# Kernel optimization log

Measured on AMD Instinct MI355X. Metric: run time of the kernel, lower is better.

Reference implementation:

```python
import jax, jax.numpy as jnp
import numpy as np
import math

E = 2048         # n_embd
H = 16           # num query head pairs (num_heads)
HKV = 8          # num_kv_heads
NREP = H // HKV  # 2
HD = E // H // 2 # head_dim = 64
DEPTH = 12
LAMBDA_INIT = 0.8 - 0.6 * math.exp(-0.3 * DEPTH)
EPS = 1e-6


def setup_inputs() -> dict:
    key = jax.random.key(0)
    ks = jax.random.split(key, 10)
    s = lambda fan_in: 1.0 / np.sqrt(fan_in)
    return {
        "x": jax.random.normal(ks[0], (2, 2048, E), jnp.float32),
        "Wq": jax.random.normal(ks[1], (E, E), jnp.float32) * s(E),
        "Wk": jax.random.normal(ks[2], (E, E // NREP), jnp.float32) * s(E),
        "Wv": jax.random.normal(ks[3], (E, E // NREP), jnp.float32) * s(E),
        "Wo": jax.random.normal(ks[4], (E, E), jnp.float32) * s(E),
        "lam_q1": jax.random.normal(ks[5], (HD,), jnp.float32) * 0.1,
        "lam_k1": jax.random.normal(ks[6], (HD,), jnp.float32) * 0.1,
        "lam_q2": jax.random.normal(ks[7], (HD,), jnp.float32) * 0.1,
        "lam_k2": jax.random.normal(ks[8], (HD,), jnp.float32) * 0.1,
        "g": jnp.ones((2 * HD,), jnp.float32),  # RMSNorm weight
    }


def _rotary(x, cos, sin):
    # x: [B, T, nh, HD]; cos/sin: [T, HD//2]
    d = x.shape[-1] // 2
    x1, x2 = x[..., :d], x[..., d:]
    c = cos[None, :, None, :]
    si = sin[None, :, None, :]
    return jnp.concatenate([x1 * c + x2 * si, -x1 * si + x2 * c], axis=-1)


def reference(x, Wq, Wk, Wv, Wo, lam_q1, lam_k1, lam_q2, lam_k2, g):
    B, T, _ = x.shape
    q = (x @ Wq).reshape(B, T, 2 * H, HD)
    k = (x @ Wk).reshape(B, T, 2 * HKV, HD)
    v = (x @ Wv).reshape(B, T, HKV, 2 * HD)

    inv_freq = 1.0 / (10000.0 ** (jnp.arange(0, HD, 2, dtype=jnp.float32) / HD))
    freqs = jnp.arange(T, dtype=jnp.float32)[:, None] * inv_freq[None, :]
    cos, sin = jnp.cos(freqs), jnp.sin(freqs)
    q = _rotary(q, cos, sin)
    k = _rotary(k, cos, sin)

    q = jnp.transpose(q, (0, 2, 1, 3)) * (HD ** -0.5)   # [B, 2H, T, HD]
    k = jnp.repeat(jnp.transpose(k, (0, 2, 1, 3)), NREP, axis=1)  # [B, 2H, T, HD]
    v = jnp.repeat(jnp.transpose(v, (0, 2, 1, 3)), NREP, axis=1)  # [B, H, T, 2HD]

    scores = jnp.einsum('bhtd,bhsd->bhts', q, k)
    scores = jnp.nan_to_num(scores)
    mask = jnp.triu(jnp.full((T, T), -jnp.inf, scores.dtype), 1)
    scores = scores + mask
    p = jax.nn.softmax(scores.astype(jnp.float32), axis=-1).astype(scores.dtype)

    lam1 = jnp.exp(jnp.sum(lam_q1 * lam_k1))
    lam2 = jnp.exp(jnp.sum(lam_q2 * lam_k2))
    lam = lam1 - lam2 + LAMBDA_INIT

    p = p.reshape(B, H, 2, T, T)
    diff = p[:, :, 0] - lam * p[:, :, 1]               # [B, H, T, T]
    attn = jnp.einsum('bhts,bhsd->bhtd', diff, v)      # [B, H, T, 2HD]

    # RMSNorm over last dim (2*HD)
    attn = attn * jax.lax.rsqrt(jnp.mean(attn * attn, axis=-1, keepdims=True) + EPS) * g
    attn = attn * (1.0 - LAMBDA_INIT)
    attn = jnp.transpose(attn, (0, 2, 1, 3)).reshape(B, T, E)
    return attn @ Wo
```

## Files before the change

### kernel.cpp

```cpp
#include <hip/hip_runtime.h>

#define T_SEQ 2048

typedef __bf16 bf16x8 __attribute__((ext_vector_type(8)));
typedef float f32x4 __attribute__((ext_vector_type(4)));
typedef unsigned short u16;

__device__ __forceinline__ u16 f2b(float f) {
  unsigned u = __float_as_uint(f);
  unsigned r = 0x7fffu + ((u >> 16) & 1u);
  return (u16)((u + r) >> 16);
}
__device__ __forceinline__ float b2f(u16 v) {
  return __uint_as_float(((unsigned)v) << 16);
}
__device__ __forceinline__ f32x4 mfma16(bf16x8 a, bf16x8 b, f32x4 c) {
  return __builtin_amdgcn_mfma_f32_16x16x32_bf16(a, b, c, 0, 0, 0);
}
__device__ __forceinline__ unsigned pkhi(float lo, float hi) {
  return __builtin_amdgcn_perm(__float_as_uint(hi), __float_as_uint(lo), 0x07060302u);
}
#if defined(__has_builtin)
#if __has_builtin(__builtin_amdgcn_exp2f)
#define HAVE_RAW_EXP2 1
#endif
#endif
__device__ __forceinline__ float exp2r(float x) {
#ifdef HAVE_RAW_EXP2
  return __builtin_amdgcn_exp2f(x);
#else
  float r;
  asm("v_exp_f32 %0, %1" : "=v"(r) : "v"(x));
  return r;
#endif
}
__device__ __forceinline__ void glds16(const void* g, void* s) {
  __builtin_amdgcn_global_load_lds(
      (const __attribute__((address_space(1))) void*)(uintptr_t)g,
      (__attribute__((address_space(3))) void*)(unsigned)(uintptr_t)s, 16, 0, 0);
}

__global__ void lam_kernel(const float* __restrict__ q1, const float* __restrict__ k1,
                           const float* __restrict__ q2, const float* __restrict__ k2,
                           float* __restrict__ outp) {
  int l = threadIdx.x;
  float a = q1[l] * k1[l];
  float c = q2[l] * k2[l];
  #pragma unroll
  for (int off = 32; off > 0; off >>= 1) {
    a += __shfl_down(a, off);
    c += __shfl_down(c, off);
  }
  if (l == 0) outp[0] = expf(a) - expf(c) + 0.7836057665316244f;
}

__global__ __launch_bounds__(256) void convert_kernel(const float* __restrict__ in,
                                                      u16* __restrict__ outp, int n) {
  int i = (blockIdx.x * 256 + threadIdx.x) * 4;
  if (i >= n) return;
  float4 v = *(const float4*)(in + i);
  ushort4 pk;
  pk.x = f2b(v.x); pk.y = f2b(v.y); pk.z = f2b(v.z); pk.w = f2b(v.w);
  *(ushort4*)(outp + i) = pk;
}

__global__ __launch_bounds__(256) void transposeW_kernel(const float* __restrict__ Wq,
                                                         const float* __restrict__ Wk,
                                                         const float* __restrict__ Wv,
                                                         const float* __restrict__ Wo,
                                                         u16* __restrict__ outp) {
  __shared__ float tile[32][33];
  const int ro0 = blockIdx.y * 32;
  const int r0 = blockIdx.x * 32;
  const float* src; int C, cbase;
  if (ro0 < 2048)      { src = Wq; C = 2048; cbase = 0; }
  else if (ro0 < 3072) { src = Wk; C = 1024; cbase = 2048; }
  else if (ro0 < 4096) { src = Wv; C = 1024; cbase = 3072; }
  else                 { src = Wo; C = 2048; cbase = 4096; }
  const int cs0 = ro0 - cbase;
  const int tx = threadIdx.x & 31, ty = threadIdx.x >> 5;
  #pragma unroll
  for (int k2 = 0; k2 < 4; k2++)
    tile[ty * 4 + k2][tx] = src[(size_t)(r0 + ty * 4 + k2) * C + cs0 + tx];
  __syncthreads();
  #pragma unroll
  for (int k2 = 0; k2 < 4; k2++)
    outp[(size_t)(ro0 + ty * 4 + k2) * 2048 + r0 + tx] = f2b(tile[tx][ty * 4 + k2]);
}

template <bool OUT_BF16>
__global__ __launch_bounds__(256) void gemm128_kernel(const u16* __restrict__ A,
                                                      const u16* __restrict__ BT,
                                                      void* __restrict__ C, int N, int K) {
  __shared__ alignas(16) u16 As[128 * 64];
  __shared__ alignas(16) u16 Bs[128 * 64];
  const int tid = threadIdx.x, w = tid >> 6, lane = tid & 63;
  const int l15 = lane & 15, quad = lane >> 4;
  const int m0 = blockIdx.y * 128, n0 = blockIdx.x * 128;
  const int wm = (w >> 1) * 64, wn = (w & 1) * 64;
  const int lr = lane >> 3, slot = lane & 7, csw = slot ^ lr;
  f32x4 acc[4][4];
  #pragma unroll
  for (int mt = 0; mt < 4; mt++)
    #pragma unroll
    for (int nt = 0; nt < 4; nt++) acc[mt][nt] = (f32x4){0.f, 0.f, 0.f, 0.f};
  const u16* Ag = A + (size_t)(m0 + w * 32 + lr) * K + csw * 8;
  const u16* Bg = BT + (size_t)(n0 + w * 32 + lr) * K + csw * 8;
  u16* Asd = As + (w * 32) * 64;
  u16* Bsd = Bs + (w * 32) * 64;
  for (int kt = 0; kt < K; kt += 64) {
    #pragma unroll
    for (int i = 0; i < 4; i++) {
      glds16(Ag + kt + (size_t)(i * 8) * K, Asd + i * 512);
      glds16(Bg + kt + (size_t)(i * 8) * K, Bsd + i * 512);
    }
    __syncthreads();
    #pragma unroll
    for (int kk = 0; kk < 2; kk++) {
      bf16x8 am[4], bn[4];
      #pragma unroll
      for (int t = 0; t < 4; t++) {
        const int ra = wm + t * 16 + l15;
        am[t] = *(const bf16x8*)&As[ra * 64 + (((kk * 4 + quad) ^ (ra & 7)) << 3)];
        const int rb = wn + t * 16 + l15;
        bn[t] = *(const bf16x8*)&Bs[rb * 64 + (((kk * 4 + quad) ^ (rb & 7)) << 3)];
      }
      #pragma unroll
      for (int mt = 0; mt < 4; mt++)
        #pragma unroll
        for (int nt = 0; nt < 4; nt++) acc[mt][nt] = mfma16(am[mt], bn[nt], acc[mt][nt]);
    }
    __syncthreads();
  }
  const int row = m0 + wm + quad * 4;
  #pragma unroll
  for (int mt = 0; mt < 4; mt++) {
    #pragma unroll
    for (int nt = 0; nt < 4; nt++) {
      const int col = n0 + wn + nt * 16 + l15;
      #pragma unroll
      for (int rr = 0; rr < 4; rr++) {
        if (OUT_BF16)
          ((u16*)C)[(size_t)(row + mt * 16 + rr) * N + col] = f2b(acc[mt][nt][rr]);
        else
          ((float*)C)[(size_t)(row + mt * 16 + rr) * N + col] = acc[mt][nt][rr];
      }
    }
  }
}

#define STAGE_HALF(TILE, ROLE, BUF)                                                     \
  do {                                                                                  \
    const u16* sp_ = ((ROLE) == 0 || (ROLE) == 3 ? Ag : Bg) +                           \
                     (size_t)((ROLE) >= 2 ? 128 : 0) * K + (size_t)(TILE) * 64;         \
    u16* dp_ = ((ROLE) == 0 || (ROLE) == 3 ? &As[BUF][0] : &Bs[BUF][0]) +               \
               (((ROLE) >= 2 ? 128 : 0) + w * 8) * 64;                                  \
    glds16(sp_, dp_);                                                                   \
    glds16(sp_ + (size_t)64 * K, dp_ + 4096);                                           \
  } while (0)

#define PHASE(I, J, BUF, NEWA, NEWB, BN, STILE, SROLE, SBUF, DOVM)                      \
  do {                                                                                  \
    if (NEWA) {                                                                         \
      _Pragma("unroll") for (int u_ = 0; u_ < 4; u_++) {                                \
        const int ar_ = ((I) * 4 + u_) * 32 + wm * 16 + l15;                            \
        _Pragma("unroll") for (int kk_ = 0; kk_ < 2; kk_++)                             \
            am[u_][kk_] = *(const bf16x8*)&As[BUF][ar_ * 64 +                           \
                              (((kk_ * 4 + quad) ^ (ar_ & 7)) << 3)];                   \
      }                                                                                 \
    }                                                                                   \
    if (NEWB) {                                                                         \
      _Pragma("unroll") for (int v_ = 0; v_ < 2; v_++) {                                \
        const int br_ = ((J) * 2 + v_) * 64 + wn * 16 + l15;                            \
        _Pragma("unroll") for (int kk_ = 0; kk_ < 2; kk_++)                             \
            BN[v_][kk_] = *(const bf16x8*)&Bs[BUF][br_ * 64 +                           \
                              (((kk_ * 4 + quad) ^ (br_ & 7)) << 3)];                   \
      }                                                                                 \
    }                                                                                   \
    STAGE_HALF(STILE, SROLE, SBUF);                                                     \
    __builtin_amdgcn_s_barrier();                                                       \
    asm volatile("s_waitcnt lgkmcnt(0)" ::: "memory");                                  \
    __builtin_amdgcn_sched_barrier(0);                                                  \
    __builtin_amdgcn_s_setprio(1);                                                      \
    _Pragma("unroll") for (int u_ = 0; u_ < 4; u_++)                                    \
        _Pragma("unroll") for (int v_ = 0; v_ < 2; v_++) {                              \
      acc[(I) * 4 + u_][(J) * 2 + v_] =                                                 \
          mfma16(am[u_][0], BN[v_][0], acc[(I) * 4 + u_][(J) * 2 + v_]);                \
      acc[(I) * 4 + u_][(J) * 2 + v_] =                                                 \
          mfma16(am[u_][1], BN[v_][1], acc[(I) * 4 + u_][(J) * 2 + v_]);                \
    }                                                                                   \
    __builtin_amdgcn_s_setprio(0);                                                      \
    if (DOVM) asm volatile("s_waitcnt vmcnt(6)" ::: "memory");                          \
    __builtin_amdgcn_s_barrier();                                                       \
  } while (0)

__global__ __launch_bounds__(512, 2) void gemm256_kernel(const u16* __restrict__ A,
                                                         const u16* __restrict__ BT,
                                                         u16* __restrict__ C, int N, int K) {
  __shared__ alignas(16) u16 As[2][256 * 64];
  __shared__ alignas(16) u16 Bs[2][256 * 64];
  const int tid = threadIdx.x, w = tid >> 6, lane = tid & 63;
  const int l15 = lane & 15, quad = lane >> 4;
  const int wm = w >> 2, wn = w & 3;
  const int lr = lane >> 3, slot = lane & 7, csw = slot ^ lr;
  const int m0 = blockIdx.y * 256, n0 = blockIdx.x * 256;
  const int nkt = K >> 6;

  f32x4 acc[8][4];
  #pragma unroll
  for (int r = 0; r < 8; r++)
    #pragma unroll
    for (int s = 0; s < 4; s++) acc[r][s] = (f32x4){0.f, 0.f, 0.f, 0.f};

  const u16* Ag = A + (size_t)(m0 + w * 8 + lr) * K + csw * 8;
  const u16* Bg = BT + (size_t)(n0 + w * 8 + lr) * K + csw * 8;

  bf16x8 am[4][2], bn0[2][2], bn1[2][2];

  STAGE_HALF(0, 0, 0); STAGE_HALF(0, 1, 0); STAGE_HALF(0, 2, 0); STAGE_HALF(0, 3, 0);
  STAGE_HALF(1, 0, 1); STAGE_HALF(1, 1, 1); STAGE_HALF(1, 2, 1);
  asm volatile("s_waitcnt vmcnt(6)" ::: "memory");
  __builtin_amdgcn_s_barrier();

  #pragma unroll 1
  for (int t = 0; t < nkt; t += 2) {
    PHASE(0, 0, 0, 1, 1, bn0, t + 1, 3, 1, 0);
    PHASE(0, 1, 0, 0, 1, bn1, t + 2, 0, 0, 0);
    PHASE(1, 0, 0, 1, 0, bn0, t + 2, 1, 0, 0);
    PHASE(1, 1, 0, 0, 0, bn1, t + 2, 2, 0, 1);
    PHASE(0, 0, 1, 1, 1, bn0, t + 2, 3, 0, 0);
    PHASE(0, 1, 1, 0, 1, bn1, t + 3, 0, 1, 0);
    PHASE(1, 0, 1, 1, 0, bn0, t + 3, 1, 1, 0);
    PHASE(1, 1, 1, 0, 0, bn1, t + 3, 2, 1, 1);
  }

  const int crow = m0 + wm * 16 + quad * 4;
  const int ccol = n0 + wn * 16 + l15;
  #pragma unroll
  for (int r = 0; r < 8; r++)
    #pragma unroll
    for (int s = 0; s < 4; s++)
      #pragma unroll
      for (int rr = 0; rr < 4; rr++)
        C[(size_t)(crow + r * 32 + rr) * N + ccol + s * 64] = f2b(acc[r][s][rr]);
}

__global__ __launch_bounds__(256) void rotab_kernel(float* __restrict__ ct,
                                                    float* __restrict__ st) {
  int idx = blockIdx.x * 256 + threadIdx.x;
  int i = idx & 31, t = idx >> 5;
  float invf = exp2f(-(float)i * 0.4152410118609203f);
  float ang = (float)t * invf;
  ct[idx] = cosf(ang);
  st[idx] = sinf(ang);
}

__global__ __launch_bounds__(256) void rotary_kernel(const u16* __restrict__ qkv,
                                                     const float* __restrict__ ct,
                                                     const float* __restrict__ st,
                                                     u16* __restrict__ Qb,
                                                     u16* __restrict__ Kb, float qscale) {
  int idx = blockIdx.x * 256 + threadIdx.x;
  int i4 = (idx & 7) * 4;
  int bt = (idx >> 3) & 4095;
  int hh = idx >> 15;
  int t = bt & (T_SEQ - 1), b = bt >> 11;
  bool isq = hh < 32;
  int col = isq ? hh * 64 : 2048 + (hh - 32) * 64;
  size_t inb = (size_t)bt * 4096 + col + i4;
  ushort4 xa = *(const ushort4*)(qkv + inb);
  ushort4 xb = *(const ushort4*)(qkv + inb + 32);
  float4 c4 = *(const float4*)(ct + t * 32 + i4);
  float4 s4 = *(const float4*)(st + t * 32 + i4);
  float scale = isq ? qscale : 1.0f;
  ushort4 o1, o2;
  {
    float x1 = b2f(xa.x), x2 = b2f(xb.x);
    o1.x = f2b((x1 * c4.x + x2 * s4.x) * scale);
    o2.x = f2b((x2 * c4.x - x1 * s4.x) * scale);
  }
  {
    float x1 = b2f(xa.y), x2 = b2f(xb.y);
    o1.y = f2b((x1 * c4.y + x2 * s4.y) * scale);
    o2.y = f2b((x2 * c4.y - x1 * s4.y) * scale);
  }
  {
    float x1 = b2f(xa.z), x2 = b2f(xb.z);
    o1.z = f2b((x1 * c4.z + x2 * s4.z) * scale);
    o2.z = f2b((x2 * c4.z - x1 * s4.z) * scale);
  }
  {
    float x1 = b2f(xa.w), x2 = b2f(xb.w);
    o1.w = f2b((x1 * c4.w + x2 * s4.w) * scale);
    o2.w = f2b((x2 * c4.w - x1 * s4.w) * scale);
  }
  u16* outp = isq ? (Qb + (size_t)(b * 32 + hh) * (T_SEQ * 64))
                  : (Kb + (size_t)(b * 16 + hh - 32) * (T_SEQ * 64));
  size_t ob = (size_t)t * 64 + i4;
  *(ushort4*)(outp + ob) = o1;
  *(ushort4*)(outp + ob + 32) = o2;
}

__global__ __launch_bounds__(256) void vtrans_kernel(const u16* __restrict__ qkv,
                                                     u16* __restrict__ outp) {
  __shared__ unsigned tile[32][33];
  int bh = blockIdx.z;
  int t0 = blockIdx.x * 32, dv0 = blockIdx.y * 32;
  int tx = threadIdx.x & 31, ty = threadIdx.x >> 5;
  int bt_base = (bh >> 3) * T_SEQ;
  int col = 3072 + (bh & 7) * 128 + dv0 + tx;
  #pragma unroll
  for (int k2 = 0; k2 < 4; k2++)
    tile[ty * 4 + k2][tx] = qkv[(size_t)(bt_base + t0 + ty * 4 + k2) * 4096 + col];
  __syncthreads();
  const int stile = t0 >> 6;
  const int sold = (t0 & 63) + tx;
  const int slo = sold & 31, hb = sold >> 5;
  const int sp = hb * 32 + ((slo >> 2) & 3) * 8 + ((slo >> 4) & 1) * 4 + (slo & 3);
  #pragma unroll
  for (int k2 = 0; k2 < 4; k2++) {
    int dv = dv0 + ty * 4 + k2;
    outp[(((size_t)bh * 32 + stile) * 128 + dv) * 64 + sp] = (u16)tile[tx][ty * 4 + k2];
  }
}

__global__ __launch_bounds__(256) void attn_kernel(const u16* __restrict__ Qb,
                                                   const u16* __restrict__ Kb,
                                                   const u16* __restrict__ Vt,
                                                   const float* __restrict__ lamp,
                                                   const float* __restrict__ g,
                                                   u16* __restrict__ attn_out) {
  __shared__ alignas(16) char smem[49152];
  u16* const Ks0 = (u16*)smem;
  u16* const Vs0 = (u16*)(smem + 16384);
  u16* const Psb = (u16*)smem;
  const int pr = blockIdx.x;
  const int bh = blockIdx.y;
  const int b = bh >> 4, h = bh & 15;
  const int tid = threadIdx.x, w = tid >> 6, lane = tid & 63;
  const int l15 = lane & 15, quad = lane >> 4;
  const int lr = lane >> 3, slot = lane & 7, csw = slot ^ lr;
  const float lam = lamp[0];

  const u16* Kg = Kb + (size_t)(b * 16 + h) * (T_SEQ * 64) + (w * 16 + lr) * 64 + csw * 8;
  const u16* Vg = Vt + (size_t)(b * 8 + (h >> 1)) * (T_SEQ * 128) + w * 2048 + lr * 64 + csw * 8;
  u16* kd[2] = {Ks0 + w * 1024, Ks0 + 4096 + w * 1024};
  u16* vd[2] = {Vs0 + w * 2048, Vs0 + 8192 + w * 2048};

  #pragma unroll 1
  for (int half = 0; half < 2; half++) {
    const int tt = half ? 31 - pr : pr;
    const int qb = tt * 64 + w * 16;
    const int qglob = qb + l15;

    bf16x8 qf[2][2];
    #pragma unroll
    for (int e = 0; e < 2; e++)
      #pragma unroll
      for (int kk = 0; kk < 2; kk++)
        qf[e][kk] = *(const bf16x8*)&Qb[((size_t)(b * 32 + 2 * h + e) * T_SEQ + qb + l15) * 64 +
                                        kk * 32 + quad * 8];

    f32x4 o[2][8];
    float lsum[2] = {0.f, 0.f};
    #pragma unroll
    for (int e = 0; e < 2; e++)
      #pragma unroll
      for (int nt = 0; nt < 8; nt++) o[e][nt] = (f32x4){0.f, 0.f, 0.f, 0.f};

    {
      glds16(Kg, kd[0]); glds16(Kg + 512, kd[0] + 512);
      glds16(Vg, vd[0]); glds16(Vg + 512, vd[0] + 512);
      glds16(Vg + 1024, vd[0] + 1024); glds16(Vg + 1536, vd[0] + 1536);
    }
    __syncthreads();

    #pragma unroll 1
    for (int st = 0; st <= tt; st++) {
      const int buf = st & 1;
      const u16* Ksb = Ks0 + buf * 4096;
      const u16* Vsb = Vs0 + buf * 8192;
      if (st < tt) {
        const u16* kp = Kg + (size_t)(st + 1) * 4096;
        const u16* vp = Vg + (size_t)(st + 1) * 8192;
        glds16(kp, kd[buf ^ 1]); glds16(kp + 512, kd[buf ^ 1] + 512);
        glds16(vp, vd[buf ^ 1]); glds16(vp + 512, vd[buf ^ 1] + 512);
        glds16(vp + 1024, vd[buf ^ 1] + 1024); glds16(vp + 1536, vd[buf ^ 1] + 1536);
      }

      bf16x8 kf[4][2];
      #pragma unroll
      for (int j = 0; j < 4; j++) {
        const int rk = j * 16 + l15;
        #pragma unroll
        for (int kk = 0; kk < 2; kk++)
          kf[j][kk] = *(const bf16x8*)&Ksb[rk * 64 + (((kk * 4 + quad) ^ (rk & 7)) << 3)];
      }

      bf16x8 pa[2][2];
      #pragma unroll
      for (int e = 0; e < 2; e++) {
        f32x4 sc[4];
        __builtin_amdgcn_s_setprio(1);
        #pragma unroll
        for (int j = 0; j < 4; j++) {
          f32x4 z = {0.f, 0.f, 0.f, 0.f};
          z = mfma16(kf[j][0], qf[e][0], z);
          sc[j] = mfma16(kf[j][1], qf[e][1], z);
        }
        __builtin_amdgcn_s_setprio(0);
        if (st == tt) {
          #pragma unroll
          for (int j = 0; j < 4; j++) {
            int srow = st * 64 + j * 16 + quad * 4;
            #pragma unroll
            for (int rr = 0; rr < 4; rr++)
              if (srow + rr > qglob) sc[j][rr] = -1e30f;
          }
        }
        float ls = 0.f;
        union { unsigned u[8]; bf16x8 v[2]; } pk;
        #pragma unroll
        for (int j = 0; j < 4; j++) {
          #pragma unroll
          for (int rr = 0; rr < 4; rr++) {
            float p = exp2r(sc[j][rr]);
            sc[j][rr] = p;
            ls += p;
          }
          pk.u[j * 2] = pkhi(sc[j][0], sc[j][1]);
          pk.u[j * 2 + 1] = pkhi(sc[j][2], sc[j][3]);
        }
        pa[e][0] = pk.v[0];
        pa[e][1] = pk.v[1];
        lsum[e] += ls;
      }
      __builtin_amdgcn_s_setprio(1);
      #pragma unroll
      for (int nt = 0; nt < 8; nt++) {
        const int rv = nt * 16 + l15;
        bf16x8 vf0 = *(const bf16x8*)&Vsb[rv * 64 + ((quad ^ (rv & 7)) << 3)];
        bf16x8 vf1 = *(const bf16x8*)&Vsb[rv * 64 + (((4 + quad) ^ (rv & 7)) << 3)];
        o[0][nt] = mfma16(vf0, pa[0][0], o[0][nt]);
        o[0][nt] = mfma16(vf1, pa[0][1], o[0][nt]);
        o[1][nt] = mfma16(vf0, pa[1][0], o[1][nt]);
        o[1][nt] = mfma16(vf1, pa[1][1], o[1][nt]);
      }
      __builtin_amdgcn_s_setprio(0);
      __syncthreads();
    }

    float l0 = lsum[0], l1 = lsum[1];
    l0 += __shfl_xor(l0, 16); l0 += __shfl_xor(l0, 32);
    l1 += __shfl_xor(l1, 16); l1 += __shfl_xor(l1, 32);
    const float il0 = 1.f / l0, il1 = lam / l1;
    float ssq = 0.f;
    #pragma unroll
    for (int nt = 0; nt < 8; nt++)
      #pragma unroll
      for (int rr = 0; rr < 4; rr++) {
        float v = o[0][nt][rr] * il0 - o[1][nt][rr] * il1;
        o[0][nt][rr] = v;
        ssq += v * v;
      }
    ssq += __shfl_xor(ssq, 16);
    ssq += __shfl_xor(ssq, 32);
    const float rsc = rsqrtf(ssq * (1.f / 128.f) + 1e-6f) * 0.2163942334683756f;
    #pragma unroll
    for (int nt = 0; nt < 8; nt++) {
      float4 gv = *(const float4*)&g[nt * 16 + quad * 4];
      uint2 pk;
      pk.x = (unsigned)f2b(o[0][nt][0] * rsc * gv.x) |
             ((unsigned)f2b(o[0][nt][1] * rsc * gv.y) << 16);
      pk.y = (unsigned)f2b(o[0][nt][2] * rsc * gv.z) |
             ((unsigned)f2b(o[0][nt][3] * rsc * gv.w) << 16);
      *(uint2*)&Psb[(w * 16 + l15) * 136 + nt * 16 + quad * 4] = pk;
    }
    asm volatile("s_waitcnt lgkmcnt(0)" ::: "memory");
    __builtin_amdgcn_sched_barrier(0);
    #pragma unroll
    for (int i = 0; i < 4; i++) {
      const int r = (lane >> 4) + i * 4, c = (lane & 15) * 8;
      bf16x8 ov = *(const bf16x8*)&Psb[(w * 16 + r) * 136 + c];
      *(bf16x8*)&attn_out[(size_t)(b * T_SEQ + qb + r) * 2048 + h * 128 + c] = ov;
    }
    __syncthreads();
  }
}

extern "C" void kernel_launch(void* const* d_in, const int* in_sizes, int n_in, void* d_out,
                              int out_size, void* d_ws, size_t ws_size, hipStream_t stream) {
  const float* x = (const float*)d_in[0];
  const float* Wq = (const float*)d_in[1];
  const float* Wk = (const float*)d_in[2];
  const float* Wv = (const float*)d_in[3];
  const float* Wo = (const float*)d_in[4];
  const float* lq1 = (const float*)d_in[5];
  const float* lk1 = (const float*)d_in[6];
  const float* lq2 = (const float*)d_in[7];
  const float* lk2 = (const float*)d_in[8];
  const float* g = (const float*)d_in[9];

  char* ws = (char*)d_ws;
  u16* WT = (u16*)(ws);
  u16* xbf = (u16*)(ws + 25165824);
  u16* QKV = (u16*)(ws + 41943040);
  u16* Qb = (u16*)(ws + 75497472);
  u16* Kb = (u16*)(ws + 92274688);
  u16* Vt = (u16*)(ws + 100663296);
  u16* Attn = (u16*)(ws + 109051904);
  float* lam = (float*)(ws + 125829120);
  float* ct = (float*)(ws + 25165824);
  float* st = (float*)(ws + 25165824 + 262144);

  lam_kernel<<<1, 64, 0, stream>>>(lq1, lk1, lq2, lk2, lam);
  convert_kernel<<<8192, 256, 0, stream>>>(x, xbf, 8388608);
  transposeW_kernel<<<dim3(64, 192), 256, 0, stream>>>(Wq, Wk, Wv, Wo, WT);
  gemm256_kernel<<<dim3(16, 16), 512, 0, stream>>>(xbf, WT, QKV, 4096, 2048);
  rotab_kernel<<<256, 256, 0, stream>>>(ct, st);
  rotary_kernel<<<6144, 256, 0, stream>>>(QKV, ct, st, Qb, Kb, 0.18033688011112042f);
  vtrans_kernel<<<dim3(64, 4, 16), 256, 0, stream>>>(QKV, Vt);
  attn_kernel<<<dim3(16, 32), 256, 0, stream>>>(Qb, Kb, Vt, lam, g, Attn);
  gemm128_kernel<false><<<dim3(16, 32), 256, 0, stream>>>(Attn, WT + (size_t)4096 * 2048, d_out,
                                                          2048, 2048);
}
```

Before: 321.0 us.

## Replace output GEMM with pipelined 128x256 kernel; compute softmax row sums via MFMA

```diff
diff --git a/kernel.cpp b/kernel.cpp
--- a/kernel.cpp
+++ b/kernel.cpp
@@ -88,67 +88,6 @@
     outp[(size_t)(ro0 + ty * 4 + k2) * 2048 + r0 + tx] = f2b(tile[tx][ty * 4 + k2]);
 }
 
-template <bool OUT_BF16>
-__global__ __launch_bounds__(256) void gemm128_kernel(const u16* __restrict__ A,
-                                                      const u16* __restrict__ BT,
-                                                      void* __restrict__ C, int N, int K) {
-  __shared__ alignas(16) u16 As[128 * 64];
-  __shared__ alignas(16) u16 Bs[128 * 64];
-  const int tid = threadIdx.x, w = tid >> 6, lane = tid & 63;
-  const int l15 = lane & 15, quad = lane >> 4;
-  const int m0 = blockIdx.y * 128, n0 = blockIdx.x * 128;
-  const int wm = (w >> 1) * 64, wn = (w & 1) * 64;
-  const int lr = lane >> 3, slot = lane & 7, csw = slot ^ lr;
-  f32x4 acc[4][4];
-  #pragma unroll
-  for (int mt = 0; mt < 4; mt++)
-    #pragma unroll
-    for (int nt = 0; nt < 4; nt++) acc[mt][nt] = (f32x4){0.f, 0.f, 0.f, 0.f};
-  const u16* Ag = A + (size_t)(m0 + w * 32 + lr) * K + csw * 8;
-  const u16* Bg = BT + (size_t)(n0 + w * 32 + lr) * K + csw * 8;
-  u16* Asd = As + (w * 32) * 64;
-  u16* Bsd = Bs + (w * 32) * 64;
-  for (int kt = 0; kt < K; kt += 64) {
-    #pragma unroll
-    for (int i = 0; i < 4; i++) {
-      glds16(Ag + kt + (size_t)(i * 8) * K, Asd + i * 512);
-      glds16(Bg + kt + (size_t)(i * 8) * K, Bsd + i * 512);
-    }
-    __syncthreads();
-    #pragma unroll
-    for (int kk = 0; kk < 2; kk++) {
-      bf16x8 am[4], bn[4];
-      #pragma unroll
-      for (int t = 0; t < 4; t++) {
-        const int ra = wm + t * 16 + l15;
-        am[t] = *(const bf16x8*)&As[ra * 64 + (((kk * 4 + quad) ^ (ra & 7)) << 3)];
-        const int rb = wn + t * 16 + l15;
-        bn[t] = *(const bf16x8*)&Bs[rb * 64 + (((kk * 4 + quad) ^ (rb & 7)) << 3)];
-      }
-      #pragma unroll
-      for (int mt = 0; mt < 4; mt++)
-        #pragma unroll
-        for (int nt = 0; nt < 4; nt++) acc[mt][nt] = mfma16(am[mt], bn[nt], acc[mt][nt]);
-    }
-    __syncthreads();
-  }
-  const int row = m0 + wm + quad * 4;
-  #pragma unroll
-  for (int mt = 0; mt < 4; mt++) {
-    #pragma unroll
-    for (int nt = 0; nt < 4; nt++) {
-      const int col = n0 + wn + nt * 16 + l15;
-      #pragma unroll
-      for (int rr = 0; rr < 4; rr++) {
-        if (OUT_BF16)
-          ((u16*)C)[(size_t)(row + mt * 16 + rr) * N + col] = f2b(acc[mt][nt][rr]);
-        else
-          ((float*)C)[(size_t)(row + mt * 16 + rr) * N + col] = acc[mt][nt][rr];
-      }
-    }
-  }
-}
-
 #define STAGE_HALF(TILE, ROLE, BUF)                                                     \
   do {                                                                                  \
     const u16* sp_ = ((ROLE) == 0 || (ROLE) == 3 ? Ag : Bg) +                           \
@@ -243,6 +182,98 @@
       #pragma unroll
       for (int rr = 0; rr < 4; rr++)
         C[(size_t)(crow + r * 32 + rr) * N + ccol + s * 64] = f2b(acc[r][s][rr]);
+}
+
+#define OSTAGE(TILE, CH, BUF)                                                           \
+  do {                                                                                  \
+    if ((CH) == 0) {                                                                    \
+      glds16(Ag + (size_t)(TILE) * 64, &As[BUF][0] + w * 512);                          \
+      glds16(Ag + (size_t)64 * K + (size_t)(TILE) * 64, &As[BUF][4096] + w * 512);      \
+      glds16(Bg + (size_t)(TILE) * 64, &Bs[BUF][0] + w * 512);                          \
+    } else {                                                                            \
+      glds16(Bg + (size_t)64 * K + (size_t)(TILE) * 64, &Bs[BUF][4096] + w * 512);      \
+      glds16(Bg + (size_t)128 * K + (size_t)(TILE) * 64, &Bs[BUF][8192] + w * 512);     \
+      glds16(Bg + (size_t)192 * K + (size_t)(TILE) * 64, &Bs[BUF][12288] + w * 512);    \
+    }                                                                                   \
+  } while (0)
+
+#define OPHASE(BUF, J, NEWA, STILE, SCH, SBUF, DOVM)                                    \
+  do {                                                                                  \
+    if (NEWA) {                                                                         \
+      _Pragma("unroll") for (int fr_ = 0; fr_ < 4; fr_++) {                             \
+        const int ar_ = wm * 64 + fr_ * 16 + l15;                                       \
+        _Pragma("unroll") for (int kk_ = 0; kk_ < 2; kk_++)                             \
+            am[fr_][kk_] = *(const bf16x8*)&As[BUF][ar_ * 64 +                          \
+                               (((kk_ * 4 + quad) ^ (ar_ & 7)) << 3)];                  \
+      }                                                                                 \
+    }                                                                                   \
+    _Pragma("unroll") for (int v_ = 0; v_ < 2; v_++) {                                  \
+      const int br_ = ((J) * 2 + v_) * 64 + wn * 16 + l15;                              \
+      _Pragma("unroll") for (int kk_ = 0; kk_ < 2; kk_++)                               \
+          bn[v_][kk_] = *(const bf16x8*)&Bs[BUF][br_ * 64 +                             \
+                            (((kk_ * 4 + quad) ^ (br_ & 7)) << 3)];                     \
+    }                                                                                   \
+    OSTAGE(STILE, SCH, SBUF);                                                           \
+    __builtin_amdgcn_s_barrier();                                                       \
+    asm volatile("s_waitcnt lgkmcnt(0)" ::: "memory");                                  \
+    __builtin_amdgcn_sched_barrier(0);                                                  \
+    __builtin_amdgcn_s_setprio(1);                                                      \
+    _Pragma("unroll") for (int fr_ = 0; fr_ < 4; fr_++)                                 \
+        _Pragma("unroll") for (int v_ = 0; v_ < 2; v_++) {                              \
+      acc[fr_][(J) * 2 + v_] = mfma16(am[fr_][0], bn[v_][0], acc[fr_][(J) * 2 + v_]);   \
+      acc[fr_][(J) * 2 + v_] = mfma16(am[fr_][1], bn[v_][1], acc[fr_][(J) * 2 + v_]);   \
+    }                                                                                   \
+    __builtin_amdgcn_s_setprio(0);                                                      \
+    if (DOVM) asm volatile("s_waitcnt vmcnt(3)" ::: "memory");                          \
+    __builtin_amdgcn_s_barrier();                                                       \
+  } while (0)
+
+__global__ __launch_bounds__(512, 2) void gemm128x256_kernel(const u16* __restrict__ A,
+                                                             const u16* __restrict__ BT,
+                                                             float* __restrict__ C,
+                                                             int N, int K) {
+  __shared__ alignas(16) u16 As[2][128 * 64];
+  __shared__ alignas(16) u16 Bs[2][256 * 64];
+  const int tid = threadIdx.x, w = tid >> 6, lane = tid & 63;
+  const int l15 = lane & 15, quad = lane >> 4;
+  const int wm = w >> 2, wn = w & 3;
+  const int lr = lane >> 3, slot = lane & 7, csw = slot ^ lr;
+  const int m0 = blockIdx.y * 128, n0 = blockIdx.x * 256;
+  const int nkt = K >> 6;
+
+  f32x4 acc[4][4];
+  #pragma unroll
+  for (int r = 0; r < 4; r++)
+    #pragma unroll
+    for (int s = 0; s < 4; s++) acc[r][s] = (f32x4){0.f, 0.f, 0.f, 0.f};
+
+  const u16* Ag = A + (size_t)(m0 + w * 8 + lr) * K + csw * 8;
+  const u16* Bg = BT + (size_t)(n0 + w * 8 + lr) * K + csw * 8;
+
+  bf16x8 am[4][2], bn[2][2];
+
+  OSTAGE(0, 0, 0); OSTAGE(0, 1, 0); OSTAGE(1, 0, 1);
+  asm volatile("s_waitcnt vmcnt(3)" ::: "memory");
+  __builtin_amdgcn_s_barrier();
+
+  #pragma unroll 1
+  for (int t = 0; t < nkt; t += 2) {
+    OPHASE(0, 0, 1, t + 1, 1, 1, 0);
+    OPHASE(0, 1, 0, t + 2, 0, 0, 1);
+    OPHASE(1, 0, 1, t + 2, 1, 0, 0);
+    OPHASE(1, 1, 0, t + 3, 0, 1, 1);
+  }
+
+  const int crow = m0 + wm * 64 + quad * 4;
+  #pragma unroll
+  for (int r = 0; r < 4; r++)
+    #pragma unroll
+    for (int s = 0; s < 4; s++) {
+      const int col = n0 + s * 64 + wn * 16 + l15;
+      #pragma unroll
+      for (int rr = 0; rr < 4; rr++)
+        C[(size_t)(crow + r * 16 + rr) * N + col] = acc[r][s][rr];
+    }
 }
 
 __global__ __launch_bounds__(256) void rotab_kernel(float* __restrict__ ct,
@@ -342,6 +373,11 @@
   const int lr = lane >> 3, slot = lane & 7, csw = slot ^ lr;
   const float lam = lamp[0];
 
+  union { unsigned u[4]; bf16x8 v; } onesu;
+  onesu.u[0] = 0x3F803F80u; onesu.u[1] = 0x3F803F80u;
+  onesu.u[2] = 0x3F803F80u; onesu.u[3] = 0x3F803F80u;
+  const bf16x8 vone = onesu.v;
+
   const u16* Kg = Kb + (size_t)(b * 16 + h) * (T_SEQ * 64) + (w * 16 + lr) * 64 + csw * 8;
   const u16* Vg = Vt + (size_t)(b * 8 + (h >> 1)) * (T_SEQ * 128) + w * 2048 + lr * 64 + csw * 8;
   u16* kd[2] = {Ks0 + w * 1024, Ks0 + 4096 + w * 1024};
@@ -362,11 +398,13 @@
                                         kk * 32 + quad * 8];
 
     f32x4 o[2][8];
-    float lsum[2] = {0.f, 0.f};
-    #pragma unroll
-    for (int e = 0; e < 2; e++)
+    f32x4 lacc[2];
+    #pragma unroll
+    for (int e = 0; e < 2; e++) {
+      lacc[e] = (f32x4){0.f, 0.f, 0.f, 0.f};
       #pragma unroll
       for (int nt = 0; nt < 8; nt++) o[e][nt] = (f32x4){0.f, 0.f, 0.f, 0.f};
+    }
 
     {
       glds16(Kg, kd[0]); glds16(Kg + 512, kd[0] + 512);
@@ -418,22 +456,18 @@
               if (srow + rr > qglob) sc[j][rr] = -1e30f;
           }
         }
-        float ls = 0.f;
         union { unsigned u[8]; bf16x8 v[2]; } pk;
         #pragma unroll
         for (int j = 0; j < 4; j++) {
           #pragma unroll
-          for (int rr = 0; rr < 4; rr++) {
-            float p = exp2r(sc[j][rr]);
-            sc[j][rr] = p;
-            ls += p;
-          }
+          for (int rr = 0; rr < 4; rr++) sc[j][rr] = exp2r(sc[j][rr]);
           pk.u[j * 2] = pkhi(sc[j][0], sc[j][1]);
           pk.u[j * 2 + 1] = pkhi(sc[j][2], sc[j][3]);
         }
         pa[e][0] = pk.v[0];
         pa[e][1] = pk.v[1];
-        lsum[e] += ls;
+        lacc[e] = mfma16(vone, pa[e][0], lacc[e]);
+        lacc[e] = mfma16(vone, pa[e][1], lacc[e]);
       }
       __builtin_amdgcn_s_setprio(1);
       #pragma unroll
@@ -450,10 +484,7 @@
       __syncthreads();
     }
 
-    float l0 = lsum[0], l1 = lsum[1];
-    l0 += __shfl_xor(l0, 16); l0 += __shfl_xor(l0, 32);
-    l1 += __shfl_xor(l1, 16); l1 += __shfl_xor(l1, 32);
-    const float il0 = 1.f / l0, il1 = lam / l1;
+    const float il0 = 1.f / lacc[0][0], il1 = lam / lacc[1][0];
     float ssq = 0.f;
     #pragma unroll
     for (int nt = 0; nt < 8; nt++)
@@ -521,6 +552,6 @@
   rotary_kernel<<<6144, 256, 0, stream>>>(QKV, ct, st, Qb, Kb, 0.18033688011112042f);
   vtrans_kernel<<<dim3(64, 4, 16), 256, 0, stream>>>(QKV, Vt);
   attn_kernel<<<dim3(16, 32), 256, 0, stream>>>(Qb, Kb, Vt, lam, g, Attn);
-  gemm128_kernel<false><<<dim3(16, 32), 256, 0, stream>>>(Attn, WT + (size_t)4096 * 2048, d_out,
-                                                          2048, 2048);
-}
+  gemm128x256_kernel<<<dim3(8, 32), 512, 0, stream>>>(Attn, WT + (size_t)4096 * 2048,
+                                                      (float*)d_out, 2048, 2048);
+}
```

After: 313.6 us. 1.02x faster.
